# Performance work log

Hardware: AMD Instinct MI355X
Metric: run time of the kernel (lower is better)

## Reference

```python
import jax, jax.numpy as jnp
import numpy as np

N = 250_000   # total instances
D = 128       # instance latent dim
F = 512       # raw instance feature dim
B = 5000      # number of bags


def setup_inputs() -> dict:
    key = jax.random.key(0)
    ks = jax.random.split(key, 7)
    z_ins = jax.random.normal(ks[0], (N, D), dtype=jnp.float32)
    bag_idx = jnp.sort(jax.random.randint(ks[1], (N,), 0, B, dtype=jnp.int32))
    bag_instances = jax.random.normal(ks[2], (N, F), dtype=jnp.float32)
    instance_mu = jax.random.normal(ks[3], (N, D), dtype=jnp.float32)
    instance_std = jax.random.uniform(ks[4], (N, D), dtype=jnp.float32)
    W = jax.random.normal(ks[5], (D, 1), dtype=jnp.float32) * 0.05
    b = jnp.zeros((1,), dtype=jnp.float32)
    return {"z_ins": z_ins, "bag_idx": bag_idx, "bag_instances": bag_instances,
            "instance_mu": instance_mu, "instance_std": instance_std,
            "W": W, "b": b}


def reference(z_ins, bag_idx, bag_instances, instance_mu, instance_std, W, b):
    # loc_ins = fc_ins(z_ins): [N, 1]
    loc_ins = z_ins @ W + b
    loc = loc_ins[:, 0]  # [N]

    # Segmented max over bags; argmax gather (first max index, matching torch.max).
    seg_max = jax.ops.segment_max(loc, bag_idx, num_segments=B)          # [B]
    is_max = loc == seg_max[bag_idx]                                     # [N]
    cand = jnp.where(is_max, jnp.arange(N, dtype=jnp.int32), N)
    arg = jax.ops.segment_min(cand, bag_idx, num_segments=B)            # [B]
    empty = arg >= N                                                     # bags with no instances stay zero
    arg_c = jnp.minimum(arg, N - 1)

    def gather(x):
        return jnp.where(empty[:, None], jnp.zeros((), x.dtype), x[arg_c])

    M = gather(loc_ins)                       # [B, 1]
    max_z_ins = gather(z_ins)                 # [B, D]
    max_instances = gather(bag_instances)     # [B, F]
    max_instances_mu = gather(instance_mu)    # [B, D]
    max_instances_std = gather(instance_std)  # [B, D]
    return (M, max_instances, max_z_ins, loc_ins, max_instances_mu, max_instances_std)
```

## Files before the change

kernel.cpp:

```cpp
#include <hip/hip_runtime.h>

#define DD 128
#define FF 512
#define BAGS 5000

__device__ __forceinline__ unsigned fkey(float f) {
    unsigned u = __float_as_uint(f);
    return (u & 0x80000000u) ? ~u : (u | 0x80000000u);
}
__device__ __forceinline__ float fkey_inv(unsigned k) {
    unsigned u = (k & 0x80000000u) ? (k & 0x7FFFFFFFu) : ~k;
    return __uint_as_float(u);
}

__global__ __launch_bounds__(256) void fused_bag_kernel(
    const float* __restrict__ z, const int* __restrict__ bag,
    const float* __restrict__ inst, const float* __restrict__ mu,
    const float* __restrict__ stdv, const float* __restrict__ W,
    const float* __restrict__ b,
    float* __restrict__ oM, float* __restrict__ oInst, float* __restrict__ oZ,
    float* __restrict__ oMu, float* __restrict__ oStd, float* __restrict__ loc,
    int N)
{
    __shared__ int s_se[2];
    __shared__ unsigned long long s_best[8];

    int bagi = blockIdx.x;
    if (threadIdx.x < 2) {
        int target = bagi + (int)threadIdx.x;
        int lo = 0, hi = N;
        while (lo < hi) {
            int mid = (lo + hi) >> 1;
            if (bag[mid] < target) lo = mid + 1; else hi = mid;
        }
        s_se[threadIdx.x] = lo;
    }
    __syncthreads();
    int s = s_se[0], e = s_se[1];

    int lane = threadIdx.x & 31;
    int grp  = threadIdx.x >> 5;
    float4 wv = ((const float4*)W)[lane];
    float bb = b[0];

    unsigned long long best = 0ull;
    for (int r = s + grp; r < e; r += 8) {
        float4 zv = ((const float4*)(z + (long long)r * DD))[lane];
        float sd = fmaf(zv.x, wv.x, fmaf(zv.y, wv.y, fmaf(zv.z, wv.z, zv.w * wv.w)));
        #pragma unroll
        for (int off = 16; off >= 1; off >>= 1) sd += __shfl_xor(sd, off, 32);
        if (lane == 0) {
            sd += bb;
            loc[r] = sd;
            unsigned long long key =
                ((unsigned long long)fkey(sd) << 32) | (unsigned)(N - 1 - r);
            if (key > best) best = key;
        }
    }
    if (lane == 0) s_best[grp] = best;
    __syncthreads();
    if (threadIdx.x == 0) {
        unsigned long long m = s_best[0];
        #pragma unroll
        for (int g = 1; g < 8; ++g) if (s_best[g] > m) m = s_best[g];
        s_best[0] = m;
    }
    __syncthreads();

    unsigned long long p = s_best[0];
    bool empty = (e <= s);
    long long ac = empty ? 0 : (long long)(N - 1 - (int)(unsigned)(p & 0xFFFFFFFFull));
    const float4 zero4 = make_float4(0.f, 0.f, 0.f, 0.f);
    int t = threadIdx.x;
    if (t < 128) {
        float4 v = empty ? zero4 : ((const float4*)(inst + ac * FF))[t];
        ((float4*)(oInst + (long long)bagi * FF))[t] = v;
    } else if (t < 160) {
        int k = t - 128;
        float4 v = empty ? zero4 : ((const float4*)(z + ac * DD))[k];
        ((float4*)(oZ + (long long)bagi * DD))[k] = v;
    } else if (t < 192) {
        int k = t - 160;
        float4 v = empty ? zero4 : ((const float4*)(mu + ac * DD))[k];
        ((float4*)(oMu + (long long)bagi * DD))[k] = v;
    } else if (t < 224) {
        int k = t - 192;
        float4 v = empty ? zero4 : ((const float4*)(stdv + ac * DD))[k];
        ((float4*)(oStd + (long long)bagi * DD))[k] = v;
    } else if (t == 224) {
        oM[bagi] = empty ? 0.f : fkey_inv((unsigned)(p >> 32));
    }
}

extern "C" void kernel_launch(void* const* d_in, const int* in_sizes, int n_in,
                              void* d_out, int out_size, void* d_ws, size_t ws_size,
                              hipStream_t stream) {
    const float* z    = (const float*)d_in[0];
    const int*   bag  = (const int*)d_in[1];
    const float* inst = (const float*)d_in[2];
    const float* mu   = (const float*)d_in[3];
    const float* stdv = (const float*)d_in[4];
    const float* W    = (const float*)d_in[5];
    const float* b    = (const float*)d_in[6];
    int N = in_sizes[1];

    float* out = (float*)d_out;
    long long off_inst = BAGS;
    long long off_z    = off_inst + (long long)BAGS * FF;
    long long off_loc  = off_z    + (long long)BAGS * DD;
    long long off_mu   = off_loc  + N;
    long long off_std  = off_mu   + (long long)BAGS * DD;

    fused_bag_kernel<<<BAGS, 256, 0, stream>>>(
        z, bag, inst, mu, stdv, W, b,
        out, out + off_inst, out + off_z, out + off_mu, out + off_std,
        out + off_loc, N);
}
```

Baseline: 44.04 us.

## Assign four lanes per row for the GEMV and reduce argmax with wave64 shuffles

Each row of z is now handled by four lanes that each load eight float4s, replacing the old 32-lane group per row (half a wave64). One block processes 64 rows per iteration instead of 8, and only a 2-step shuffle is needed per row. The per-wave argmax is then combined with shuffle-down over the 64-lane wave before the shared-memory combine. The aim is more rows in flight per block and less shuffle overhead. The cost is more registers per thread for the W slices, and each lane's loads are strided rather than contiguous within a row.

Measured after the change: 44.87 us. Within noise of the previous version (+1.9%).

```diff
diff --git a/kernel.cpp b/kernel.cpp
--- a/kernel.cpp
+++ b/kernel.cpp
@@ -23,7 +23,7 @@
     int N)
 {
     __shared__ int s_se[2];
-    __shared__ unsigned long long s_best[8];
+    __shared__ unsigned long long s_best[4];
 
     int bagi = blockIdx.x;
     if (threadIdx.x < 2) {
@@ -35,34 +35,56 @@
         }
         s_se[threadIdx.x] = lo;
     }
+
+    int tid  = threadIdx.x;
+    int lane = tid & 63;
+    int wave = tid >> 6;
+    int ll   = lane & 3;
+    int rowslot = lane >> 4 == 0 ? (lane >> 2) : (lane >> 2);
+    int rslot = wave * 16 + (lane >> 2);
+
+    float4 wk[8];
+    #pragma unroll
+    for (int j = 0; j < 8; ++j) wk[j] = ((const float4*)W)[ll + 4 * j];
+    float bb = b[0];
+
     __syncthreads();
     int s = s_se[0], e = s_se[1];
 
-    int lane = threadIdx.x & 31;
-    int grp  = threadIdx.x >> 5;
-    float4 wv = ((const float4*)W)[lane];
-    float bb = b[0];
-
     unsigned long long best = 0ull;
-    for (int r = s + grp; r < e; r += 8) {
-        float4 zv = ((const float4*)(z + (long long)r * DD))[lane];
-        float sd = fmaf(zv.x, wv.x, fmaf(zv.y, wv.y, fmaf(zv.z, wv.z, zv.w * wv.w)));
+    for (long long row = s + rslot; row < e; row += 64) {
+        const float4* zr = (const float4*)(z + row * DD);
+        float4 acc = make_float4(0.f, 0.f, 0.f, 0.f);
         #pragma unroll
-        for (int off = 16; off >= 1; off >>= 1) sd += __shfl_xor(sd, off, 32);
-        if (lane == 0) {
-            sd += bb;
-            loc[r] = sd;
+        for (int j = 0; j < 8; ++j) {
+            float4 zv = zr[ll + 4 * j];
+            acc.x = fmaf(zv.x, wk[j].x, acc.x);
+            acc.y = fmaf(zv.y, wk[j].y, acc.y);
+            acc.z = fmaf(zv.z, wk[j].z, acc.z);
+            acc.w = fmaf(zv.w, wk[j].w, acc.w);
+        }
+        float sd = (acc.x + acc.y) + (acc.z + acc.w);
+        sd += __shfl_xor(sd, 1, 64);
+        sd += __shfl_xor(sd, 2, 64);
+        sd += bb;
+        if (ll == 0) {
+            loc[row] = sd;
             unsigned long long key =
-                ((unsigned long long)fkey(sd) << 32) | (unsigned)(N - 1 - r);
+                ((unsigned long long)fkey(sd) << 32) | (unsigned)(N - 1 - (int)row);
             if (key > best) best = key;
         }
     }
-    if (lane == 0) s_best[grp] = best;
+    #pragma unroll
+    for (int off = 4; off <= 32; off <<= 1) {
+        unsigned long long o = __shfl_down(best, off, 64);
+        if (o > best) best = o;
+    }
+    if (lane == 0) s_best[wave] = best;
     __syncthreads();
-    if (threadIdx.x == 0) {
+    if (tid == 0) {
         unsigned long long m = s_best[0];
         #pragma unroll
-        for (int g = 1; g < 8; ++g) if (s_best[g] > m) m = s_best[g];
+        for (int g = 1; g < 4; ++g) if (s_best[g] > m) m = s_best[g];
         s_best[0] = m;
     }
     __syncthreads();
```
